# Kernel optimization log

Hardware: AMD Instinct MI355X
Metric: run time of the kernel (lower is better)

Reference implementation:

```python
import jax, jax.numpy as jnp
import numpy as np

TEMP = 0.05
EPS = 1e-6


def _l2norm(x):
    return x / jnp.linalg.norm(x, axis=1, keepdims=True)


def setup_inputs() -> dict:
    key = jax.random.key(0)
    k1, k2, k3, k4 = jax.random.split(key, 4)
    B, D = 4096, 768
    return {
        "feat": jax.random.normal(k1, (B, D), dtype=jnp.float32),
        "feat_gen": jax.random.normal(k2, (B, D), dtype=jnp.float32),
        "feat_aug": jax.random.normal(k3, (B, D), dtype=jnp.float32),
        "targets": jax.random.randint(k4, (B,), 0, 100, dtype=jnp.int64),
    }


def reference(feat, feat_gen, feat_aug, targets):
    B = feat.shape[0]
    on = _l2norm(feat)
    gn = _l2norm(feat_gen)
    an = _l2norm(feat_aug)
    # [B, B] exp-similarity matrices
    exp_ori = jnp.exp(on @ on.T / TEMP)
    exp_gen = jnp.exp(on @ gn.T / TEMP)
    exp_aug = jnp.exp(on @ an.T / TEMP)

    same = (targets[:, None] == targets[None, :])  # [B, B] bool, includes diagonal
    same_f = same.astype(exp_ori.dtype)

    # ---- co loss: anchors vs ori+aug columns ----
    oa = exp_ori + exp_aug
    diff_sum_oa = oa.sum(axis=1) - (oa * same_f).sum(axis=1)        # [B]
    denom_co = diff_sum_oa + exp_gen.sum(axis=1) + EPS              # [B]
    term_o = -jnp.log(exp_ori / (exp_ori + denom_co[:, None]) + EPS)
    term_a = -jnp.log(exp_aug / (exp_aug + denom_co[:, None]) + EPS)
    co_loss = ((term_o + term_a) * same_f).sum() / B

    # ---- ad loss: anchors vs gen columns ----
    diff_sum_g = exp_gen.sum(axis=1) - (exp_gen * same_f).sum(axis=1)
    denom_ad = diff_sum_g + exp_aug.sum(axis=1) + exp_ori.sum(axis=1) + EPS
    term_g = -jnp.log(exp_gen / (exp_gen + denom_ad[:, None]) + EPS)
    ad_loss = (term_g * same_f).sum() / B

    return (ad_loss, co_loss)
```

## Files before the change

### kernel.cpp

```cpp
#include <hip/hip_runtime.h>
#include <hip/hip_bf16.h>
#include <math.h>

#define Bn 4096
#define Dd 768
#define SC2 28.85390081777927f
#define EPSF 1e-6f
#define DG 4.8516519541e8f

#define O_S      0
#define O_SMOA   12288
#define O_SMG    16384
#define ZERO_F   20480
#define O_P      20480
#define O_RM     20608
#define LIST_OFF   262144
#define LCAP       (1u << 19)
#define NB_OFF     33554432

typedef __attribute__((ext_vector_type(8))) short sh8;
typedef __attribute__((ext_vector_type(4))) float f32x4;

#define AS1 __attribute__((address_space(1)))
#define AS3 __attribute__((address_space(3)))

static __device__ __forceinline__ void gl_lds16(const void* g, void* l) {
    __builtin_amdgcn_global_load_lds((const AS1 void*)g, (AS3 void*)l, 16, 0, 0);
}

static __device__ __forceinline__ unsigned short f2b(float f) {
    unsigned int u = __float_as_uint(f);
    unsigned int r = (u + 0x7fffu + ((u >> 16) & 1u)) >> 16;
    return (unsigned short)r;
}

__global__ void norm_sort_kernel(const float* f0, const float* f1, const float* f2,
                                 unsigned short* nb, const int* tg, unsigned int* I,
                                 float* out) {
    int r = blockIdx.x, m = blockIdx.y, tid = threadIdx.x;
    if (r == Bn) {
        if (m != 0) return;
        float* F = (float*)I;
        __shared__ unsigned int h[128], pb[128], cur[128];
        for (int e = tid; e < ZERO_F; e += 256) F[e] = 0.f;
        if (tid == 0) { out[0] = 0.f; out[1] = 0.f; }
        if (tid < 128) { h[tid] = 0; cur[tid] = 0; }
        __syncthreads();
        for (int e = tid; e < Bn; e += 256) atomicAdd(&h[tg[e]], 1u);
        __syncthreads();
        if (tid < 128) pb[tid] = h[tid] * h[tid];
        __syncthreads();
        for (int s = 1; s < 128; s <<= 1) {
            unsigned int b = 0;
            if (tid < 128 && tid >= s) b = pb[tid - s];
            __syncthreads();
            if (tid < 128) pb[tid] += b;
            __syncthreads();
        }
        if (tid == 127) I[O_P] = pb[127];
        uint2* RM = (uint2*)(I + O_RM);
        for (int e = tid; e < Bn; e += 256) {
            int c = tg[e];
            unsigned int rk = atomicAdd(&cur[c], 1u);
            unsigned int n = h[c];
            RM[e] = make_uint2((unsigned)c | (rk << 8), (pb[c] - n * n) + rk * n);
        }
        return;
    }
    const float* src = (m == 0 ? f0 : (m == 1 ? f1 : f2)) + (size_t)r * Dd;
    float x0 = src[tid], x1 = src[tid + 256], x2 = src[tid + 512];
    float v = x0 * x0 + x1 * x1 + x2 * x2;
    #pragma unroll
    for (int off = 1; off < 64; off <<= 1) v += __shfl_xor(v, off);
    __shared__ float wr[4];
    if ((tid & 63) == 0) wr[tid >> 6] = v;
    __syncthreads();
    float inv = rsqrtf(wr[0] + wr[1] + wr[2] + wr[3]);
    unsigned short* dst = nb + ((size_t)m * Bn + r) * Dd;
    dst[tid] = f2b(x0 * inv);
    dst[tid + 256] = f2b(x1 * inv);
    dst[tid + 512] = f2b(x2 * inv);
}

__launch_bounds__(256, 2)
__global__ void gemm_rowsum(const unsigned short* nb, char* ws) {
    float* F = (float*)ws;
    const unsigned int* I = (const unsigned int*)ws;
    const uint2* RM = (const uint2*)(I + O_RM);
    int bid = blockIdx.x;
    int xcd = bid & 7, local = bid >> 3;
    int n0 = (xcd * 4 + (local & 3)) * 128;
    int m0 = (local >> 2) * 128;
    int tid = threadIdx.x, lane = tid & 63, wave = tid >> 6;
    int wm = (wave >> 1) * 64, wn = (wave & 1) * 64;
    int lid = lane & 15, q = lane >> 4;
    __shared__ __align__(16) unsigned short Asm[128 * 32];
    __shared__ __align__(16) unsigned short Bsm[3][128 * 32];

    int row0 = tid >> 2, ch = tid & 3;
    int cs = (ch ^ ((row0 >> 1) & 3)) * 8;
    const unsigned short* gA  = nb + (size_t)(m0 + row0) * Dd + cs;
    const unsigned short* gB0 = nb + (size_t)(n0 + row0) * Dd + cs;
    const unsigned short* gB1 = gB0 + (size_t)Bn * Dd;
    const unsigned short* gB2 = gB1 + (size_t)Bn * Dd;
    unsigned short* lA0 = &Asm[tid * 8];
    unsigned short* lA1 = &Asm[(tid + 256) * 8];

    int cswz = (q ^ ((lid >> 1) & 3)) * 8;

    f32x4 a0[4][4] = {}, a1[4][4] = {}, a2[4][4] = {};

    for (int kt = 0; kt < 24; ++kt) {
        const unsigned short* pa  = gA  + kt * 32;
        const unsigned short* pb0 = gB0 + kt * 32;
        const unsigned short* pb1 = gB1 + kt * 32;
        const unsigned short* pb2 = gB2 + kt * 32;
        __syncthreads();
        gl_lds16(pa, lA0);
        gl_lds16(pa + (size_t)64 * Dd, lA1);
        gl_lds16(pb0, &Bsm[0][tid * 8]);
        gl_lds16(pb0 + (size_t)64 * Dd, &Bsm[0][(tid + 256) * 8]);
        gl_lds16(pb1, &Bsm[1][tid * 8]);
        gl_lds16(pb1 + (size_t)64 * Dd, &Bsm[1][(tid + 256) * 8]);
        gl_lds16(pb2, &Bsm[2][tid * 8]);
        gl_lds16(pb2 + (size_t)64 * Dd, &Bsm[2][(tid + 256) * 8]);
        __syncthreads();
        sh8 af[4], bf0[4], bf1[4], bf2[4];
        #pragma unroll
        for (int i = 0; i < 4; ++i)
            af[i] = *(const sh8*)&Asm[(wm + i * 16 + lid) * 32 + cswz];
        #pragma unroll
        for (int j = 0; j < 4; ++j)
            bf0[j] = *(const sh8*)&Bsm[0][(wn + j * 16 + lid) * 32 + cswz];
        #pragma unroll
        for (int j = 0; j < 4; ++j)
            bf1[j] = *(const sh8*)&Bsm[1][(wn + j * 16 + lid) * 32 + cswz];
        __builtin_amdgcn_sched_barrier(0);
        __builtin_amdgcn_s_setprio(1);
        #pragma unroll
        for (int i = 0; i < 4; ++i)
            #pragma unroll
            for (int j = 0; j < 4; ++j)
                a0[i][j] = __builtin_amdgcn_mfma_f32_16x16x32_bf16(af[i], bf0[j], a0[i][j], 0, 0, 0);
        __builtin_amdgcn_s_setprio(0);
        __builtin_amdgcn_sched_barrier(0);
        #pragma unroll
        for (int j = 0; j < 4; ++j)
            bf2[j] = *(const sh8*)&Bsm[2][(wn + j * 16 + lid) * 32 + cswz];
        __builtin_amdgcn_sched_barrier(0);
        __builtin_amdgcn_s_setprio(1);
        #pragma unroll
        for (int i = 0; i < 4; ++i)
            #pragma unroll
            for (int j = 0; j < 4; ++j)
                a1[i][j] = __builtin_amdgcn_mfma_f32_16x16x32_bf16(af[i], bf1[j], a1[i][j], 0, 0, 0);
        __builtin_amdgcn_s_setprio(0);
        __builtin_amdgcn_sched_barrier(0);
        __builtin_amdgcn_s_setprio(1);
        #pragma unroll
        for (int i = 0; i < 4; ++i)
            #pragma unroll
            for (int j = 0; j < 4; ++j)
                a2[i][j] = __builtin_amdgcn_mfma_f32_16x16x32_bf16(af[i], bf2[j], a2[i][j], 0, 0, 0);
        __builtin_amdgcn_s_setprio(0);
    }

    uint2 rmc[4];
    #pragma unroll
    for (int j = 0; j < 4; ++j) rmc[j] = RM[n0 + wn + j * 16 + lid];
    uint4* Lq = (uint4*)(ws + LIST_OFF);
    #pragma unroll
    for (int i = 0; i < 4; ++i)
        #pragma unroll
        for (int reg = 0; reg < 4; ++reg) {
            int grow = m0 + wm + i * 16 + q * 4 + reg;
            uint2 rm = RM[grow];
            unsigned int trow = rm.x & 255u, rsb = rm.y;
            float rs0 = 0.f, rs1 = 0.f, rs2 = 0.f, msOA = 0.f, msG = 0.f;
            #pragma unroll
            for (int j = 0; j < 4; ++j) {
                int gcol = n0 + wn + j * 16 + lid;
                float x0 = a0[i][j][reg] * SC2;
                float x1 = a1[i][j][reg] * SC2;
                float x2 = a2[i][j][reg] * SC2;
                float e0 = exp2f(x0);
                float e1 = exp2f(x1);
                float e2 = exp2f(x2);
                if (gcol == grow) e0 = 0.f;
                rs0 += e0; rs1 += e1; rs2 += e2;
                if ((rmc[j].x & 255u) == trow) {
                    msOA += e0 + e2;
                    msG  += e1;
                    unsigned int slot = rsb + (rmc[j].x >> 8);
                    if (slot < LCAP)
                        Lq[slot] = make_uint4((unsigned)grow, __float_as_uint(x0),
                                              __float_as_uint(x1), __float_as_uint(x2));
                }
            }
            #pragma unroll
            for (int off = 1; off < 16; off <<= 1) {
                rs0 += __shfl_xor(rs0, off);
                rs1 += __shfl_xor(rs1, off);
                rs2 += __shfl_xor(rs2, off);
                msOA += __shfl_xor(msOA, off);
                msG  += __shfl_xor(msG, off);
            }
            if (lid == 0) {
                atomicAdd(&F[O_S + grow], rs0);
                atomicAdd(&F[O_S + Bn + grow], rs1);
                atomicAdd(&F[O_S + 2 * Bn + grow], rs2);
                atomicAdd(&F[O_SMOA + grow], msOA);
                atomicAdd(&F[O_SMG + grow], msG);
            }
        }
}

__launch_bounds__(256)
__global__ void loss_kernel(char* ws, float* out) {
    float* F = (float*)ws;
    const unsigned int* I = (const unsigned int*)ws;
    const uint4* L = (const uint4*)(ws + LIST_OFF);
    unsigned int n = I[O_P]; if (n > LCAP) n = LCAP;
    float a0 = 0.f, a1 = 0.f;
    unsigned int stride = gridDim.x * 256;
    for (unsigned int idx = blockIdx.x * 256 + threadIdx.x; idx < n; idx += stride) {
        uint4 en = L[idx];
        int i = (int)en.x;
        float son = F[O_S + i], sgen = F[O_S + Bn + i], saug = F[O_S + 2 * Bn + i];
        float dco = (son + saug - F[O_SMOA + i]) + sgen + EPSF;
        float dad = (sgen - F[O_SMG + i]) + saug + son + DG + EPSF;
        float eo = exp2f(__uint_as_float(en.y));
        float eg = exp2f(__uint_as_float(en.z));
        float ea = exp2f(__uint_as_float(en.w));
        a0 += -__logf(eg / (eg + dad) + EPSF);
        a1 += -__logf(eo / (eo + dco) + EPSF) - __logf(ea / (ea + dco) + EPSF);
    }
    #pragma unroll
    for (int off = 1; off < 64; off <<= 1) { a0 += __shfl_xor(a0, off); a1 += __shfl_xor(a1, off); }
    __shared__ float r0[4], r1[4];
    int tid = threadIdx.x;
    if ((tid & 63) == 0) { r0[tid >> 6] = a0; r1[tid >> 6] = a1; }
    __syncthreads();
    if (tid == 0) {
        atomicAdd(&out[0], (r0[0] + r0[1] + r0[2] + r0[3]) * (1.0f / Bn));
        atomicAdd(&out[1], (r1[0] + r1[1] + r1[2] + r1[3]) * (1.0f / Bn));
    }
}

extern "C" void kernel_launch(void* const* d_in, const int* in_sizes, int n_in,
                              void* d_out, int out_size, void* d_ws, size_t ws_size,
                              hipStream_t stream) {
    const float* f0 = (const float*)d_in[0];
    const float* f1 = (const float*)d_in[1];
    const float* f2 = (const float*)d_in[2];
    const int* tg = (const int*)d_in[3];
    char* ws = (char*)d_ws;
    unsigned int* I = (unsigned int*)d_ws;
    unsigned short* nb = (unsigned short*)(ws + NB_OFF);
    float* out = (float*)d_out;

    norm_sort_kernel<<<dim3(Bn + 1, 3), 256, 0, stream>>>(f0, f1, f2, nb, tg, I, out);
    gemm_rowsum<<<dim3(1024), 256, 0, stream>>>(nb, ws);
    loss_kernel<<<256, 256, 0, stream>>>(ws, out);
}
```

Measured before the change: 201.5 us.

## Double-buffer LDS tiles in the triple GEMM to prefetch the next k-slice

```diff
diff --git a/kernel.cpp b/kernel.cpp
--- a/kernel.cpp
+++ b/kernel.cpp
@@ -94,8 +94,7 @@
     int tid = threadIdx.x, lane = tid & 63, wave = tid >> 6;
     int wm = (wave >> 1) * 64, wn = (wave & 1) * 64;
     int lid = lane & 15, q = lane >> 4;
-    __shared__ __align__(16) unsigned short Asm[128 * 32];
-    __shared__ __align__(16) unsigned short Bsm[3][128 * 32];
+    __shared__ __align__(16) unsigned short L[2][4][128 * 32];
 
     int row0 = tid >> 2, ch = tid & 3;
     int cs = (ch ^ ((row0 >> 1) & 3)) * 8;
@@ -103,38 +102,45 @@
     const unsigned short* gB0 = nb + (size_t)(n0 + row0) * Dd + cs;
     const unsigned short* gB1 = gB0 + (size_t)Bn * Dd;
     const unsigned short* gB2 = gB1 + (size_t)Bn * Dd;
-    unsigned short* lA0 = &Asm[tid * 8];
-    unsigned short* lA1 = &Asm[(tid + 256) * 8];
 
     int cswz = (q ^ ((lid >> 1) & 3)) * 8;
 
     f32x4 a0[4][4] = {}, a1[4][4] = {}, a2[4][4] = {};
 
+#define STAGE(b, kt) { \
+    const unsigned short* pa  = gA  + (kt) * 32; \
+    const unsigned short* pb0 = gB0 + (kt) * 32; \
+    const unsigned short* pb1 = gB1 + (kt) * 32; \
+    const unsigned short* pb2 = gB2 + (kt) * 32; \
+    gl_lds16(pa, &L[b][0][tid * 8]); \
+    gl_lds16(pa + (size_t)64 * Dd, &L[b][0][(tid + 256) * 8]); \
+    gl_lds16(pb0, &L[b][1][tid * 8]); \
+    gl_lds16(pb0 + (size_t)64 * Dd, &L[b][1][(tid + 256) * 8]); \
+    gl_lds16(pb1, &L[b][2][tid * 8]); \
+    gl_lds16(pb1 + (size_t)64 * Dd, &L[b][2][(tid + 256) * 8]); \
+    gl_lds16(pb2, &L[b][3][tid * 8]); \
+    gl_lds16(pb2 + (size_t)64 * Dd, &L[b][3][(tid + 256) * 8]); \
+}
+
+    STAGE(0, 0);
+    __syncthreads();
+
     for (int kt = 0; kt < 24; ++kt) {
-        const unsigned short* pa  = gA  + kt * 32;
-        const unsigned short* pb0 = gB0 + kt * 32;
-        const unsigned short* pb1 = gB1 + kt * 32;
-        const unsigned short* pb2 = gB2 + kt * 32;
-        __syncthreads();
-        gl_lds16(pa, lA0);
-        gl_lds16(pa + (size_t)64 * Dd, lA1);
-        gl_lds16(pb0, &Bsm[0][tid * 8]);
-        gl_lds16(pb0 + (size_t)64 * Dd, &Bsm[0][(tid + 256) * 8]);
-        gl_lds16(pb1, &Bsm[1][tid * 8]);
-        gl_lds16(pb1 + (size_t)64 * Dd, &Bsm[1][(tid + 256) * 8]);
-        gl_lds16(pb2, &Bsm[2][tid * 8]);
-        gl_lds16(pb2 + (size_t)64 * Dd, &Bsm[2][(tid + 256) * 8]);
-        __syncthreads();
+        int p = kt & 1;
+        if (kt < 23) {
+            STAGE(p ^ 1, kt + 1);
+            __builtin_amdgcn_sched_barrier(0);
+        }
         sh8 af[4], bf0[4], bf1[4], bf2[4];
         #pragma unroll
         for (int i = 0; i < 4; ++i)
-            af[i] = *(const sh8*)&Asm[(wm + i * 16 + lid) * 32 + cswz];
+            af[i] = *(const sh8*)&L[p][0][(wm + i * 16 + lid) * 32 + cswz];
         #pragma unroll
         for (int j = 0; j < 4; ++j)
-            bf0[j] = *(const sh8*)&Bsm[0][(wn + j * 16 + lid) * 32 + cswz];
+            bf0[j] = *(const sh8*)&L[p][1][(wn + j * 16 + lid) * 32 + cswz];
         #pragma unroll
         for (int j = 0; j < 4; ++j)
-            bf1[j] = *(const sh8*)&Bsm[1][(wn + j * 16 + lid) * 32 + cswz];
+            bf1[j] = *(const sh8*)&L[p][2][(wn + j * 16 + lid) * 32 + cswz];
         __builtin_amdgcn_sched_barrier(0);
         __builtin_amdgcn_s_setprio(1);
         #pragma unroll
@@ -146,7 +152,7 @@
         __builtin_amdgcn_sched_barrier(0);
         #pragma unroll
         for (int j = 0; j < 4; ++j)
-            bf2[j] = *(const sh8*)&Bsm[2][(wn + j * 16 + lid) * 32 + cswz];
+            bf2[j] = *(const sh8*)&L[p][3][(wn + j * 16 + lid) * 32 + cswz];
         __builtin_amdgcn_sched_barrier(0);
         __builtin_amdgcn_s_setprio(1);
         #pragma unroll
@@ -163,6 +169,7 @@
             for (int j = 0; j < 4; ++j)
                 a2[i][j] = __builtin_amdgcn_mfma_f32_16x16x32_bf16(af[i], bf2[j], a2[i][j], 0, 0, 0);
         __builtin_amdgcn_s_setprio(0);
+        if (kt < 23) __syncthreads();
     }
 
     uint2 rmc[4];
```

Measured after the change: 200.1 us. No clear change (-0.7%).

## Load GEMM operand fragments directly from global memory instead of LDS staging

Applied to the files above, without the earlier changes.

```diff
diff --git a/kernel.cpp b/kernel.cpp
--- a/kernel.cpp
+++ b/kernel.cpp
@@ -20,13 +20,6 @@
 
 typedef __attribute__((ext_vector_type(8))) short sh8;
 typedef __attribute__((ext_vector_type(4))) float f32x4;
-
-#define AS1 __attribute__((address_space(1)))
-#define AS3 __attribute__((address_space(3)))
-
-static __device__ __forceinline__ void gl_lds16(const void* g, void* l) {
-    __builtin_amdgcn_global_load_lds((const AS1 void*)g, (AS3 void*)l, 16, 0, 0);
-}
 
 static __device__ __forceinline__ unsigned short f2b(float f) {
     unsigned int u = __float_as_uint(f);
@@ -94,69 +87,40 @@
     int tid = threadIdx.x, lane = tid & 63, wave = tid >> 6;
     int wm = (wave >> 1) * 64, wn = (wave & 1) * 64;
     int lid = lane & 15, q = lane >> 4;
-    __shared__ __align__(16) unsigned short Asm[128 * 32];
-    __shared__ __align__(16) unsigned short Bsm[3][128 * 32];
-
-    int row0 = tid >> 2, ch = tid & 3;
-    int cs = (ch ^ ((row0 >> 1) & 3)) * 8;
-    const unsigned short* gA  = nb + (size_t)(m0 + row0) * Dd + cs;
-    const unsigned short* gB0 = nb + (size_t)(n0 + row0) * Dd + cs;
-    const unsigned short* gB1 = gB0 + (size_t)Bn * Dd;
-    const unsigned short* gB2 = gB1 + (size_t)Bn * Dd;
-    unsigned short* lA0 = &Asm[tid * 8];
-    unsigned short* lA1 = &Asm[(tid + 256) * 8];
-
-    int cswz = (q ^ ((lid >> 1) & 3)) * 8;
+
+    const unsigned short* pA  = nb + (size_t)(m0 + wm + lid) * Dd + q * 8;
+    const unsigned short* pB0 = nb + (size_t)(n0 + wn + lid) * Dd + q * 8;
+    const unsigned short* pB1 = pB0 + (size_t)Bn * Dd;
+    const unsigned short* pB2 = pB1 + (size_t)Bn * Dd;
 
     f32x4 a0[4][4] = {}, a1[4][4] = {}, a2[4][4] = {};
 
     for (int kt = 0; kt < 24; ++kt) {
-        const unsigned short* pa  = gA  + kt * 32;
-        const unsigned short* pb0 = gB0 + kt * 32;
-        const unsigned short* pb1 = gB1 + kt * 32;
-        const unsigned short* pb2 = gB2 + kt * 32;
-        __syncthreads();
-        gl_lds16(pa, lA0);
-        gl_lds16(pa + (size_t)64 * Dd, lA1);
-        gl_lds16(pb0, &Bsm[0][tid * 8]);
-        gl_lds16(pb0 + (size_t)64 * Dd, &Bsm[0][(tid + 256) * 8]);
-        gl_lds16(pb1, &Bsm[1][tid * 8]);
-        gl_lds16(pb1 + (size_t)64 * Dd, &Bsm[1][(tid + 256) * 8]);
-        gl_lds16(pb2, &Bsm[2][tid * 8]);
-        gl_lds16(pb2 + (size_t)64 * Dd, &Bsm[2][(tid + 256) * 8]);
-        __syncthreads();
+        int ko = kt * 32;
         sh8 af[4], bf0[4], bf1[4], bf2[4];
         #pragma unroll
         for (int i = 0; i < 4; ++i)
-            af[i] = *(const sh8*)&Asm[(wm + i * 16 + lid) * 32 + cswz];
+            af[i] = *(const sh8*)(pA + (size_t)i * 16 * Dd + ko);
         #pragma unroll
         for (int j = 0; j < 4; ++j)
-            bf0[j] = *(const sh8*)&Bsm[0][(wn + j * 16 + lid) * 32 + cswz];
+            bf0[j] = *(const sh8*)(pB0 + (size_t)j * 16 * Dd + ko);
         #pragma unroll
         for (int j = 0; j < 4; ++j)
-            bf1[j] = *(const sh8*)&Bsm[1][(wn + j * 16 + lid) * 32 + cswz];
-        __builtin_amdgcn_sched_barrier(0);
+            bf1[j] = *(const sh8*)(pB1 + (size_t)j * 16 * Dd + ko);
+        #pragma unroll
+        for (int j = 0; j < 4; ++j)
+            bf2[j] = *(const sh8*)(pB2 + (size_t)j * 16 * Dd + ko);
         __builtin_amdgcn_s_setprio(1);
         #pragma unroll
         for (int i = 0; i < 4; ++i)
             #pragma unroll
             for (int j = 0; j < 4; ++j)
                 a0[i][j] = __builtin_amdgcn_mfma_f32_16x16x32_bf16(af[i], bf0[j], a0[i][j], 0, 0, 0);
-        __builtin_amdgcn_s_setprio(0);
-        __builtin_amdgcn_sched_barrier(0);
-        #pragma unroll
-        for (int j = 0; j < 4; ++j)
-            bf2[j] = *(const sh8*)&Bsm[2][(wn + j * 16 + lid) * 32 + cswz];
-        __builtin_amdgcn_sched_barrier(0);
-        __builtin_amdgcn_s_setprio(1);
         #pragma unroll
         for (int i = 0; i < 4; ++i)
             #pragma unroll
             for (int j = 0; j < 4; ++j)
                 a1[i][j] = __builtin_amdgcn_mfma_f32_16x16x32_bf16(af[i], bf1[j], a1[i][j], 0, 0, 0);
-        __builtin_amdgcn_s_setprio(0);
-        __builtin_amdgcn_sched_barrier(0);
-        __builtin_amdgcn_s_setprio(1);
         #pragma unroll
         for (int i = 0; i < 4; ++i)
             #pragma unroll
```

After: 308.5 us. 53.1% more time.

## Switch GEMM to single-wave 64x64 tiles with barrier-free prefetch of next K-slice

Applied to the files above, without the earlier changes.

```diff
diff --git a/kernel.cpp b/kernel.cpp
--- a/kernel.cpp
+++ b/kernel.cpp
@@ -82,104 +82,96 @@
     dst[tid + 512] = f2b(x2 * inv);
 }
 
-__launch_bounds__(256, 2)
+__launch_bounds__(64, 2)
 __global__ void gemm_rowsum(const unsigned short* nb, char* ws) {
     float* F = (float*)ws;
     const unsigned int* I = (const unsigned int*)ws;
     const uint2* RM = (const uint2*)(I + O_RM);
     int bid = blockIdx.x;
     int xcd = bid & 7, local = bid >> 3;
-    int n0 = (xcd * 4 + (local & 3)) * 128;
-    int m0 = (local >> 2) * 128;
-    int tid = threadIdx.x, lane = tid & 63, wave = tid >> 6;
-    int wm = (wave >> 1) * 64, wn = (wave & 1) * 64;
+    int n0 = (xcd * 8 + (local & 7)) * 64;
+    int m0 = (local >> 3) * 64;
+    int lane = threadIdx.x;
     int lid = lane & 15, q = lane >> 4;
-    __shared__ __align__(16) unsigned short Asm[128 * 32];
-    __shared__ __align__(16) unsigned short Bsm[3][128 * 32];
-
-    int row0 = tid >> 2, ch = tid & 3;
+    __shared__ __align__(16) unsigned short L[4][2048];
+
+    int row0 = lane >> 2, ch = lane & 3;
     int cs = (ch ^ ((row0 >> 1) & 3)) * 8;
     const unsigned short* gA  = nb + (size_t)(m0 + row0) * Dd + cs;
     const unsigned short* gB0 = nb + (size_t)(n0 + row0) * Dd + cs;
     const unsigned short* gB1 = gB0 + (size_t)Bn * Dd;
     const unsigned short* gB2 = gB1 + (size_t)Bn * Dd;
-    unsigned short* lA0 = &Asm[tid * 8];
-    unsigned short* lA1 = &Asm[(tid + 256) * 8];
 
     int cswz = (q ^ ((lid >> 1) & 3)) * 8;
 
     f32x4 a0[4][4] = {}, a1[4][4] = {}, a2[4][4] = {};
 
+#define STG(kt) { int ko = (kt) * 32; \
+    _Pragma("unroll") \
+    for (int g = 0; g < 4; ++g) { \
+        gl_lds16(gA  + (size_t)g * 16 * Dd + ko, &L[0][g * 512]); \
+        gl_lds16(gB0 + (size_t)g * 16 * Dd + ko, &L[1][g * 512]); \
+        gl_lds16(gB1 + (size_t)g * 16 * Dd + ko, &L[2][g * 512]); \
+        gl_lds16(gB2 + (size_t)g * 16 * Dd + ko, &L[3][g * 512]); } }
+
+    STG(0);
     for (int kt = 0; kt < 24; ++kt) {
-        const unsigned short* pa  = gA  + kt * 32;
-        const unsigned short* pb0 = gB0 + kt * 32;
-        const unsigned short* pb1 = gB1 + kt * 32;
-        const unsigned short* pb2 = gB2 + kt * 32;
-        __syncthreads();
-        gl_lds16(pa, lA0);
-        gl_lds16(pa + (size_t)64 * Dd, lA1);
-        gl_lds16(pb0, &Bsm[0][tid * 8]);
-        gl_lds16(pb0 + (size_t)64 * Dd, &Bsm[0][(tid + 256) * 8]);
-        gl_lds16(pb1, &Bsm[1][tid * 8]);
-        gl_lds16(pb1 + (size_t)64 * Dd, &Bsm[1][(tid + 256) * 8]);
-        gl_lds16(pb2, &Bsm[2][tid * 8]);
-        gl_lds16(pb2 + (size_t)64 * Dd, &Bsm[2][(tid + 256) * 8]);
-        __syncthreads();
-        sh8 af[4], bf0[4], bf1[4], bf2[4];
-        #pragma unroll
-        for (int i = 0; i < 4; ++i)
-            af[i] = *(const sh8*)&Asm[(wm + i * 16 + lid) * 32 + cswz];
+        asm volatile("s_waitcnt vmcnt(0)" ::: "memory");
+        __builtin_amdgcn_sched_barrier(0);
+        sh8 af[4], bfA[4], bfB[4];
+        #pragma unroll
+        for (int i = 0; i < 4; ++i)
+            af[i] = *(const sh8*)&L[0][(i * 16 + lid) * 32 + cswz];
         #pragma unroll
         for (int j = 0; j < 4; ++j)
-            bf0[j] = *(const sh8*)&Bsm[0][(wn + j * 16 + lid) * 32 + cswz];
+            bfA[j] = *(const sh8*)&L[1][(j * 16 + lid) * 32 + cswz];
+        __builtin_amdgcn_s_setprio(1);
+        #pragma unroll
+        for (int i = 0; i < 4; ++i)
+            #pragma unroll
+            for (int j = 0; j < 4; ++j)
+                a0[i][j] = __builtin_amdgcn_mfma_f32_16x16x32_bf16(af[i], bfA[j], a0[i][j], 0, 0, 0);
+        __builtin_amdgcn_s_setprio(0);
         #pragma unroll
         for (int j = 0; j < 4; ++j)
-            bf1[j] = *(const sh8*)&Bsm[1][(wn + j * 16 + lid) * 32 + cswz];
+            bfB[j] = *(const sh8*)&L[2][(j * 16 + lid) * 32 + cswz];
+        __builtin_amdgcn_s_setprio(1);
+        #pragma unroll
+        for (int i = 0; i < 4; ++i)
+            #pragma unroll
+            for (int j = 0; j < 4; ++j)
+                a1[i][j] = __builtin_amdgcn_mfma_f32_16x16x32_bf16(af[i], bfB[j], a1[i][j], 0, 0, 0);
+        __builtin_amdgcn_s_setprio(0);
+        #pragma unroll
+        for (int j = 0; j < 4; ++j)
+            bfA[j] = *(const sh8*)&L[3][(j * 16 + lid) * 32 + cswz];
+        asm volatile("s_waitcnt lgkmcnt(0)" ::: "memory");
         __builtin_amdgcn_sched_barrier(0);
+        if (kt < 23) STG(kt + 1);
         __builtin_amdgcn_s_setprio(1);
         #pragma unroll
         for (int i = 0; i < 4; ++i)
             #pragma unroll
             for (int j = 0; j < 4; ++j)
-                a0[i][j] = __builtin_amdgcn_mfma_f32_16x16x32_bf16(af[i], bf0[j], a0[i][j], 0, 0, 0);
+                a2[i][j] = __builtin_amdgcn_mfma_f32_16x16x32_bf16(af[i], bfA[j], a2[i][j], 0, 0, 0);
         __builtin_amdgcn_s_setprio(0);
-        __builtin_amdgcn_sched_barrier(0);
-        #pragma unroll
-        for (int j = 0; j < 4; ++j)
-            bf2[j] = *(const sh8*)&Bsm[2][(wn + j * 16 + lid) * 32 + cswz];
-        __builtin_amdgcn_sched_barrier(0);
-        __builtin_amdgcn_s_setprio(1);
-        #pragma unroll
-        for (int i = 0; i < 4; ++i)
-            #pragma unroll
-            for (int j = 0; j < 4; ++j)
-                a1[i][j] = __builtin_amdgcn_mfma_f32_16x16x32_bf16(af[i], bf1[j], a1[i][j], 0, 0, 0);
-        __builtin_amdgcn_s_setprio(0);
-        __builtin_amdgcn_sched_barrier(0);
-        __builtin_amdgcn_s_setprio(1);
-        #pragma unroll
-        for (int i = 0; i < 4; ++i)
-            #pragma unroll
-            for (int j = 0; j < 4; ++j)
-                a2[i][j] = __builtin_amdgcn_mfma_f32_16x16x32_bf16(af[i], bf2[j], a2[i][j], 0, 0, 0);
-        __builtin_amdgcn_s_setprio(0);
     }
 
     uint2 rmc[4];
     #pragma unroll
-    for (int j = 0; j < 4; ++j) rmc[j] = RM[n0 + wn + j * 16 + lid];
+    for (int j = 0; j < 4; ++j) rmc[j] = RM[n0 + j * 16 + lid];
     uint4* Lq = (uint4*)(ws + LIST_OFF);
     #pragma unroll
     for (int i = 0; i < 4; ++i)
         #pragma unroll
         for (int reg = 0; reg < 4; ++reg) {
-            int grow = m0 + wm + i * 16 + q * 4 + reg;
+            int grow = m0 + i * 16 + q * 4 + reg;
             uint2 rm = RM[grow];
             unsigned int trow = rm.x & 255u, rsb = rm.y;
             float rs0 = 0.f, rs1 = 0.f, rs2 = 0.f, msOA = 0.f, msG = 0.f;
             #pragma unroll
             for (int j = 0; j < 4; ++j) {
-                int gcol = n0 + wn + j * 16 + lid;
+                int gcol = n0 + j * 16 + lid;
                 float x0 = a0[i][j][reg] * SC2;
                 float x1 = a1[i][j][reg] * SC2;
                 float x2 = a2[i][j][reg] * SC2;
@@ -260,6 +252,6 @@
     float* out = (float*)d_out;
 
     norm_sort_kernel<<<dim3(Bn + 1, 3), 256, 0, stream>>>(f0, f1, f2, nb, tg, I, out);
-    gemm_rowsum<<<dim3(1024), 256, 0, stream>>>(nb, ws);
+    gemm_rowsum<<<dim3(4096), 64, 0, stream>>>(nb, ws);
     loss_kernel<<<256, 256, 0, stream>>>(ws, out);
 }
```

New measurement: 226.2 us. 12.3% more time.
